# Performance work log

Measured on AMD Instinct MI355X. Metric: run time of the kernel, lower is better.

The kernel has to match this reference:

```python
import jax, jax.numpy as jnp
import numpy as np
from jax import lax

K_TOP = 4
NF1, NF2 = 6, 14
KS1, KS2 = 7, 5


def conv1d_grouped(x, w, b, groups, pad):
    # x: (B, Cin, L), w: (Cout, Cin//groups, K)
    y = lax.conv_general_dilated(x, w, window_strides=(1,), padding=[(pad, pad)],
                                 dimension_numbers=('NCH', 'OIH', 'NCH'),
                                 feature_group_count=groups)
    return y + b[None, :, None]


def kmax_pool(x, k):
    # order-preserving k-max along last axis
    idx = jnp.sort(lax.top_k(x, k)[1], axis=-1)
    return jnp.take_along_axis(x, idx, axis=-1)


def fold_sum(h, b, nf, rows, L):
    # h: (B, rows*nf, L) with group-major channel layout (rows groups of nf)
    h = h.reshape(b, rows, nf, L).transpose(0, 2, 1, 3)        # (B, nf, rows, L)
    h = h.reshape(b, nf, rows // 2, 2, L).sum(axis=3)          # Fold(2,2): sum adjacent row pairs
    return h.transpose(0, 2, 1, 3).reshape(b, (rows // 2) * nf, L)


def setup_inputs() -> dict:
    key = jax.random.key(0)
    ks = jax.random.split(key, 8)
    V, D, C, B, S = 50257, 256, 1000, 32, 1024
    x = jax.random.randint(ks[0], (B, S), 0, V)
    emb = jax.random.normal(ks[1], (V, D), jnp.float32)
    w1 = jax.random.normal(ks[2], (NF1 * D, 1, KS1), jnp.float32) * 0.1
    b1 = jnp.zeros((NF1 * D,), jnp.float32)
    w2 = jax.random.normal(ks[3], (NF2 * (D // 2), NF1, KS2), jnp.float32) * 0.05
    b2 = jnp.zeros((NF2 * (D // 2),), jnp.float32)
    wf = jax.random.normal(ks[4], (C, NF2 * (D // 4) * K_TOP), jnp.float32) * 0.02
    bf = jnp.zeros((C,), jnp.float32)
    return {"x": x, "emb": emb, "w1": w1, "b1": b1, "w2": w2, "b2": b2, "wf": wf, "bf": bf}


def reference(x, emb, w1, b1, w2, b2, wf, bf):
    D = emb.shape[1]
    B = x.shape[0]
    h = emb[x].transpose(0, 2, 1)                 # (B, D, S)
    h = conv1d_grouped(h, w1, b1, groups=D, pad=KS1 - 1)   # (B, 6D, S+6)
    L1 = h.shape[-1]
    h = fold_sum(h, B, NF1, D, L1)                # (B, 3D, L1)
    # dynamic k-max: layer 1 of 2 -> k = max(k_top, ceil(L/2))
    k1 = max(K_TOP, -(-L1 // 2))
    h = jnp.tanh(kmax_pool(h, k1))
    h = conv1d_grouped(h, w2, b2, groups=D // 2, pad=KS2 - 1)  # (B, 7D, k1+4)
    L2 = h.shape[-1]
    h = fold_sum(h, B, NF2, D // 2, L2)           # (B, 14*(D/4), L2)
    h = jnp.tanh(kmax_pool(h, K_TOP))             # (B, 14*(D/4), k_top)
    # dropout is identity in eval mode
    h = h.reshape(B, -1)
    return h @ wf.T + bf
```

## Files before the change

kernel.cpp:

```cpp
#include <hip/hip_runtime.h>
#include <hip/hip_bf16.h>


typedef __attribute__((ext_vector_type(8))) short short8;
typedef __attribute__((ext_vector_type(4))) float f32x4;

__device__ __forceinline__ float fast_tanh(float x) {
    float e = __expf(2.f * x);
    return 1.f - 2.f / (e + 1.f);
}

__device__ __forceinline__ unsigned fkey(float f) {
    unsigned u = __float_as_uint(f);
    return (u & 0x80000000u) ? ~u : (u | 0x80000000u);
}

__device__ __forceinline__ float fkey_inv(unsigned k) {
    unsigned u = (k & 0x80000000u) ? (k ^ 0x80000000u) : ~k;
    return __uint_as_float(u);
}

__device__ __forceinline__ unsigned short f2bf_rne(float f) {
    unsigned u = __float_as_uint(f);
    return (unsigned short)((u + 0x7fffu + ((u >> 16) & 1u)) >> 16);
}

__global__ __launch_bounds__(256) void gather_kernel(
    const int* __restrict__ x, const float* __restrict__ emb, float* __restrict__ E2)
{
    const int b = blockIdx.x >> 4;
    const int c64 = blockIdx.x & 15;
    const int wv = threadIdx.x >> 6, lane = threadIdx.x & 63;
    float* dst = E2 + ((((size_t)b << 6) + lane) << 12);
#pragma unroll
    for (int t = 0; t < 16; ++t) {
        int l = (c64 << 6) + (wv << 4) + t;
        int tok = x[(b << 10) + l];
        float4 v = *(const float4*)(emb + ((size_t)tok << 8) + (lane << 2));
        *(float4*)(dst + (size_t)l * 4) = v;
    }
}

__global__ __launch_bounds__(896) void stage12_kernel(
    const int* __restrict__ x, const float* __restrict__ emb,
    const float* __restrict__ w1, const float* __restrict__ b1,
    const float* __restrict__ w2, const float* __restrict__ b2,
    const float* __restrict__ E2,
    __hip_bfloat16* __restrict__ H)
{
    __shared__ __align__(16) float e[4 * 1104];
    __shared__ __align__(16) float F[12 * 584];
    const int b = blockIdx.x >> 6;
    const int r2 = blockIdx.x & 63;
    const int tid = threadIdx.x;

    for (int i = tid; i < 12 * 584; i += 896) F[i] = 0.f;
    if (E2) {
        const float* E2blk = E2 + ((((size_t)b << 6) + r2) << 12);
        for (int idx = tid; idx < 1104; idx += 896) {
            int l = idx - 6;
            float4 v = {0.f, 0.f, 0.f, 0.f};
            if (l >= 0 && l < 1024) v = *(const float4*)(E2blk + (size_t)l * 4);
            e[0 * 1104 + idx] = v.x; e[1 * 1104 + idx] = v.y;
            e[2 * 1104 + idx] = v.z; e[3 * 1104 + idx] = v.w;
        }
    } else {
        for (int idx = tid; idx < 1104; idx += 896) {
            int l = idx - 6;
            float4 v = {0.f, 0.f, 0.f, 0.f};
            if (l >= 0 && l < 1024) {
                int tok = x[(b << 10) + l];
                v = *(const float4*)(emb + ((size_t)tok << 8) + (r2 << 2));
            }
            e[0 * 1104 + idx] = v.x; e[1 * 1104 + idx] = v.y;
            e[2 * 1104 + idx] = v.z; e[3 * 1104 + idx] = v.w;
        }
    }
    __syncthreads();

    const int w = tid >> 6;
    const int lane = tid & 63;

    if (w < 12) {
        const int half = (w >= 6) ? 1 : 0;
        const int f = w - half * 6;
        const float* ep0 = e + (2 * half) * 1104;
        const float* ep1 = ep0 + 1104;
        const int c0 = __builtin_amdgcn_readfirstlane((2 * (2 * r2 + half)) * 6 + f);
        const int c1 = c0 + 6;
        float wA[7], wB[7];
#pragma unroll
        for (int t = 0; t < 7; ++t) { wA[t] = w1[c0 * 7 + t]; wB[t] = w1[c1 * 7 + t]; }
        const float bias = b1[c0] + b1[c1];

        const int pos0 = lane * 17;
        float a0[7], a1[7];
#pragma unroll
        for (int t = 0; t < 7; ++t) { a0[t] = ep0[pos0 + t]; a1[t] = ep1[pos0 + t]; }

        unsigned key[17];
#pragma unroll
        for (int j = 0; j < 17; ++j) {
            float a = bias;
#pragma unroll
            for (int t = 0; t < 7; ++t) a += a0[t] * wA[t] + a1[t] * wB[t];
            key[j] = (pos0 + j < 1030) ? fkey(a) : 0u;
            if (j < 16) {
#pragma unroll
                for (int t = 0; t < 6; ++t) { a0[t] = a0[t + 1]; a1[t] = a1[t + 1]; }
                a0[6] = ep0[pos0 + j + 7];
                a1[6] = ep1[pos0 + j + 7];
            }
        }

        unsigned T = 0u;
        for (int bit = 31; bit >= 0; --bit) {
            unsigned cand = T | (1u << bit);
            int cnt = 0;
#pragma unroll
            for (int j = 0; j < 17; ++j) cnt += (int)__popcll(__ballot(key[j] >= cand));
            if (cnt >= 515) T = cand;
            if (cnt == 515) break;
        }

        const unsigned long long lm = (1ull << lane) - 1ull;
        int gt_tot = 0, gt_run = 0, eq_run = 0;
#pragma unroll
        for (int j = 0; j < 17; ++j) {
            unsigned long long bg = __ballot(key[j] > T);
            unsigned long long be = __ballot(key[j] == T);
            gt_tot += (int)__popcll(bg);
            gt_run += (int)__popcll(bg & lm);
            eq_run += (int)__popcll(be & lm);
        }
        const int q = 515 - gt_tot;
        float* Frow = F + w * 584;
#pragma unroll
        for (int j = 0; j < 17; ++j) {
            bool isgt = key[j] > T;
            bool iseq = key[j] == T;
            int pos = gt_run + (eq_run < q ? eq_run : q);
            if (isgt || (iseq && eq_run < q)) Frow[4 + pos] = fast_tanh(fkey_inv(key[j]));
            gt_run += isgt ? 1 : 0;
            eq_run += iseq ? 1 : 0;
        }
    }
    __syncthreads();

    {
        const int j = w;
        const int base = lane * 9;
        const int bidx = __builtin_amdgcn_readfirstlane((2 * r2) * 14 + j);
        const float bias2 = b2[bidx] + b2[bidx + 14];
        float acc[9];
#pragma unroll
        for (int jj = 0; jj < 9; ++jj) acc[jj] = bias2;

#pragma unroll
        for (int i = 0; i < 12; ++i) {
            const float* Fr = F + i * 584 + base;
            const int cg = 2 * r2 + ((i >= 6) ? 1 : 0);
            const int ii = (i >= 6) ? (i - 6) : i;
            const int widx = __builtin_amdgcn_readfirstlane(((cg * 14 + j) * 6 + ii) * 5);
            float wv[5];
#pragma unroll
            for (int t = 0; t < 5; ++t) wv[t] = w2[widx + t];
            float win[5];
#pragma unroll
            for (int t = 0; t < 5; ++t) win[t] = Fr[t];
#pragma unroll
            for (int jj = 0; jj < 9; ++jj) {
#pragma unroll
                for (int t = 0; t < 5; ++t) acc[jj] += win[t] * wv[t];
                if (jj < 8) {
#pragma unroll
                    for (int t = 0; t < 4; ++t) win[t] = win[t + 1];
                    win[4] = Fr[jj + 5];
                }
            }
        }

        float vv[9];
#pragma unroll
        for (int jj = 0; jj < 9; ++jj) vv[jj] = (base + jj < 519) ? acc[jj] : -INFINITY;
        float sv[4]; int si[4];
#pragma unroll
        for (int it = 0; it < 4; ++it) {
            float m = vv[0]; int mi = base;
#pragma unroll
            for (int jj = 1; jj < 9; ++jj) { if (vv[jj] > m) { m = vv[jj]; mi = base + jj; } }
#pragma unroll
            for (int d = 1; d < 64; d <<= 1) {
                float om = __shfl_xor(m, d, 64);
                int omi = __shfl_xor(mi, d, 64);
                if (om > m || (om == m && omi < mi)) { m = om; mi = omi; }
            }
            sv[it] = m; si[it] = mi;
            int lj = mi - base;
#pragma unroll
            for (int jj = 0; jj < 9; ++jj) if (jj == lj) vv[jj] = -INFINITY;
        }
#define CSWAP(a, bq) { if (si[a] > si[bq]) { int ti = si[a]; si[a] = si[bq]; si[bq] = ti; \
                                             float tv = sv[a]; sv[a] = sv[bq]; sv[bq] = tv; } }
        CSWAP(0, 1) CSWAP(2, 3) CSWAP(0, 2) CSWAP(1, 3) CSWAP(1, 2)
#undef CSWAP
        if (lane == 0) {
            __hip_bfloat16* op = H + (size_t)b * 3584 + (r2 * 14 + j) * 4;
#pragma unroll
            for (int k = 0; k < 4; ++k) op[k] = __float2bfloat16(fast_tanh(sv[k]));
        }
    }
}

__global__ __launch_bounds__(256) void bias_init_kernel(
    const float* __restrict__ bfv, float* __restrict__ out)
{
    int idx = blockIdx.x * 256 + threadIdx.x;
    if (idx < 32000) out[idx] = bfv[idx - (idx / 1000) * 1000];
}

__global__ __launch_bounds__(256) void stage3_kernel(
    const __hip_bfloat16* __restrict__ Hb, const float* __restrict__ wf,
    float* __restrict__ out)
{
    __shared__ __align__(16) float sred[2 * 4 * 256];
    const int nt = blockIdx.x % 63;
    const int kc = blockIdx.x / 63;
    const int w = threadIdx.x >> 6, lane = threadIdx.x & 63;
    const int row = lane & 15, quad = lane >> 4;
    const int c = nt * 16 + row;
    const bool cvalid = (c < 1000);
    const int kofs = kc * 896 + w * 224 + quad * 8;
    const __hip_bfloat16* ap0 = Hb + (size_t)row * 3584 + kofs;
    const __hip_bfloat16* ap1 = ap0 + (size_t)16 * 3584;
    const float* bp = wf + (size_t)(cvalid ? c : 0) * 3584 + kofs;

    f32x4 acc0 = {0.f, 0.f, 0.f, 0.f};
    f32x4 acc1 = {0.f, 0.f, 0.f, 0.f};
#pragma unroll
    for (int it = 0; it < 7; ++it) {
        short8 a0 = *(const short8*)(ap0 + it * 32);
        short8 a1 = *(const short8*)(ap1 + it * 32);
        float4 p0 = *(const float4*)(bp + it * 32);
        float4 p1 = *(const float4*)(bp + it * 32 + 4);
        short8 bfr;
        bfr[0] = (short)f2bf_rne(p0.x); bfr[1] = (short)f2bf_rne(p0.y);
        bfr[2] = (short)f2bf_rne(p0.z); bfr[3] = (short)f2bf_rne(p0.w);
        bfr[4] = (short)f2bf_rne(p1.x); bfr[5] = (short)f2bf_rne(p1.y);
        bfr[6] = (short)f2bf_rne(p1.z); bfr[7] = (short)f2bf_rne(p1.w);
        if (!cvalid) bfr = short8{0, 0, 0, 0, 0, 0, 0, 0};
        acc0 = __builtin_amdgcn_mfma_f32_16x16x32_bf16(a0, bfr, acc0, 0, 0, 0);
        acc1 = __builtin_amdgcn_mfma_f32_16x16x32_bf16(a1, bfr, acc1, 0, 0, 0);
    }
#pragma unroll
    for (int r_ = 0; r_ < 4; ++r_) {
        sred[(0 * 4 + w) * 256 + lane * 4 + r_] = acc0[r_];
        sred[(1 * 4 + w) * 256 + lane * 4 + r_] = acc1[r_];
    }
    __syncthreads();
    if (threadIdx.x < 128) {
        const int mt = threadIdx.x >> 6;
        const int l2 = threadIdx.x & 63;
        const int rr = l2 & 15, qq = l2 >> 4;
        const int cc = nt * 16 + rr;
        if (cc < 1000) {
            const float* sp = sred + mt * 4 * 256;
#pragma unroll
            for (int r_ = 0; r_ < 4; ++r_) {
                float s = sp[0 * 256 + l2 * 4 + r_] + sp[1 * 256 + l2 * 4 + r_]
                        + sp[2 * 256 + l2 * 4 + r_] + sp[3 * 256 + l2 * 4 + r_];
                int brow = mt * 16 + qq * 4 + r_;
                atomicAdd(&out[brow * 1000 + cc], s);
            }
        }
    }
}

extern "C" void kernel_launch(void* const* d_in, const int* in_sizes, int n_in,
                              void* d_out, int out_size, void* d_ws, size_t ws_size,
                              hipStream_t stream) {
    const int* x      = (const int*)d_in[0];
    const float* emb  = (const float*)d_in[1];
    const float* w1   = (const float*)d_in[2];
    const float* b1   = (const float*)d_in[3];
    const float* w2   = (const float*)d_in[4];
    const float* b2   = (const float*)d_in[5];
    const float* wf   = (const float*)d_in[6];
    const float* bfv  = (const float*)d_in[7];

    const size_t E2_BYTES = (size_t)32 * 64 * 1024 * 4 * 4;
    const size_t H_BYTES  = (size_t)32 * 3584 * 2;
    float* E2 = nullptr;
    __hip_bfloat16* H;
    if (ws_size >= E2_BYTES + H_BYTES) {
        E2 = (float*)d_ws;
        H = (__hip_bfloat16*)((char*)d_ws + E2_BYTES);
    } else {
        H = (__hip_bfloat16*)d_ws;
    }

    bias_init_kernel<<<125, 256, 0, stream>>>(bfv, (float*)d_out);
    if (E2) gather_kernel<<<32 * 16, 256, 0, stream>>>(x, emb, E2);
    stage12_kernel<<<32 * 64, 896, 0, stream>>>(x, emb, w1, b1, w2, b2, E2, H);
    stage3_kernel<<<63 * 4, 256, 0, stream>>>(H, wf, (float*)d_out);
}
```

Baseline: 259.8 us.

## Split fused conv/k-max stage into two kernels with global intermediate buffer

Replaces the single large 896-thread stage12 kernel with a conv1+fold+k-max-select kernel (two blocks per row pair, radix-select via ballots) that writes tanh'd selected values to a global workspace, followed by a conv2+fold+top-4 kernel that reads them back. The aim is higher occupancy and better parallelism by using smaller blocks with less shared memory. In exchange it adds a round trip through global memory for the intermediate (about 50 MB) and one more launch. It also halves the gather kernel's per-block work, and the new path runs only when the workspace is large enough.

```diff
diff --git a/kernel.cpp b/kernel.cpp
--- a/kernel.cpp
+++ b/kernel.cpp
@@ -4,6 +4,7 @@
 
 typedef __attribute__((ext_vector_type(8))) short short8;
 typedef __attribute__((ext_vector_type(4))) float f32x4;
+typedef __attribute__((ext_vector_type(2))) float v2f;
 
 __device__ __forceinline__ float fast_tanh(float x) {
     float e = __expf(2.f * x);
@@ -28,16 +29,190 @@
 __global__ __launch_bounds__(256) void gather_kernel(
     const int* __restrict__ x, const float* __restrict__ emb, float* __restrict__ E2)
 {
-    const int b = blockIdx.x >> 4;
-    const int c64 = blockIdx.x & 15;
+    const int b = blockIdx.x >> 5;
+    const int c32 = blockIdx.x & 31;
     const int wv = threadIdx.x >> 6, lane = threadIdx.x & 63;
     float* dst = E2 + ((((size_t)b << 6) + lane) << 12);
 #pragma unroll
-    for (int t = 0; t < 16; ++t) {
-        int l = (c64 << 6) + (wv << 4) + t;
+    for (int t = 0; t < 8; ++t) {
+        int l = (c32 << 5) + (wv << 3) + t;
         int tok = x[(b << 10) + l];
         float4 v = *(const float4*)(emb + ((size_t)tok << 8) + (lane << 2));
         *(float4*)(dst + (size_t)l * 4) = v;
+    }
+}
+
+__global__ __launch_bounds__(384, 8) void convsel_kernel(
+    const float* __restrict__ E2, const float* __restrict__ w1, const float* __restrict__ b1,
+    float* __restrict__ Fg)
+{
+    __shared__ __align__(8) v2f e2[1104];
+    const int b = blockIdx.x >> 7;
+    const int r2 = (blockIdx.x >> 1) & 63;
+    const int half = blockIdx.x & 1;
+    const int tid = threadIdx.x;
+
+    const float* E2blk = E2 + ((((size_t)b << 6) + r2) << 12) + 2 * half;
+    for (int idx = tid; idx < 1104; idx += 384) {
+        int l = idx - 6;
+        v2f v = {0.f, 0.f};
+        if (l >= 0 && l < 1024) {
+            float2 p = *(const float2*)(E2blk + (size_t)l * 4);
+            v = v2f{p.x, p.y};
+        }
+        e2[idx] = v;
+    }
+    __syncthreads();
+
+    const int w = tid >> 6;
+    const int lane = tid & 63;
+    const int c0 = __builtin_amdgcn_readfirstlane((2 * (2 * r2 + half)) * 6 + w);
+    const int c1 = c0 + 6;
+    v2f wp[7];
+#pragma unroll
+    for (int t = 0; t < 7; ++t) wp[t] = v2f{w1[c0 * 7 + t], w1[c1 * 7 + t]};
+    const float bias = b1[c0] + b1[c1];
+
+    const int pos0 = lane * 17;
+    v2f a01[7];
+#pragma unroll
+    for (int t = 0; t < 7; ++t) a01[t] = e2[pos0 + t];
+
+    unsigned key[17];
+#pragma unroll
+    for (int j = 0; j < 17; ++j) {
+        v2f pa = {0.f, 0.f};
+#pragma unroll
+        for (int t = 0; t < 7; ++t) pa += a01[t] * wp[t];
+        float a = bias + (pa.x + pa.y);
+        key[j] = (pos0 + j < 1030) ? fkey(a) : 0u;
+        if (j < 16) {
+#pragma unroll
+            for (int t = 0; t < 6; ++t) a01[t] = a01[t + 1];
+            a01[6] = e2[pos0 + j + 7];
+        }
+    }
+
+    unsigned T = 0u;
+    for (int bit = 31; bit >= 0; --bit) {
+        unsigned cand = T | (1u << bit);
+        int cnt = 0;
+#pragma unroll
+        for (int j = 0; j < 17; ++j) cnt += (int)__popcll(__ballot(key[j] >= cand));
+        if (cnt >= 515) T = cand;
+        if (cnt == 515) break;
+    }
+
+    const unsigned long long lm = (1ull << lane) - 1ull;
+    int gt_tot = 0, gt_run = 0, eq_run = 0;
+#pragma unroll
+    for (int j = 0; j < 17; ++j) {
+        unsigned long long bg = __ballot(key[j] > T);
+        unsigned long long be = __ballot(key[j] == T);
+        gt_tot += (int)__popcll(bg);
+        gt_run += (int)__popcll(bg & lm);
+        eq_run += (int)__popcll(be & lm);
+    }
+    const int q = 515 - gt_tot;
+    float* Frow = Fg + (size_t)(((b << 6) + r2) * 12 + (half * 6 + w)) * 515;
+#pragma unroll
+    for (int j = 0; j < 17; ++j) {
+        bool isgt = key[j] > T;
+        bool iseq = key[j] == T;
+        int pos = gt_run + (eq_run < q ? eq_run : q);
+        if (isgt || (iseq && eq_run < q)) Frow[pos] = fast_tanh(fkey_inv(key[j]));
+        gt_run += isgt ? 1 : 0;
+        eq_run += iseq ? 1 : 0;
+    }
+}
+
+__global__ __launch_bounds__(448, 7) void conv2max_kernel(
+    const float* __restrict__ Fg, const float* __restrict__ w2, const float* __restrict__ b2,
+    __hip_bfloat16* __restrict__ H)
+{
+    __shared__ __align__(16) float Fs[12 * 584];
+    const int b = blockIdx.x >> 6;
+    const int r2 = blockIdx.x & 63;
+    const int tid = threadIdx.x;
+    const float* Ft = Fg + (size_t)(((b << 6) + r2) * 12) * 515;
+
+#pragma unroll
+    for (int i = 0; i < 12; ++i) {
+        for (int pos = tid; pos < 584; pos += 448) {
+            float v = 0.f;
+            if (pos >= 4 && pos < 519) v = Ft[i * 515 + pos - 4];
+            Fs[i * 584 + pos] = v;
+        }
+    }
+    __syncthreads();
+
+    const int w = tid >> 6;
+    const int lane = tid & 63;
+
+    for (int rep = 0; rep < 2; ++rep) {
+        const int j = w + rep * 7;
+        const int base = lane * 9;
+        const int bidx = __builtin_amdgcn_readfirstlane((2 * r2) * 14 + j);
+        const float bias2 = b2[bidx] + b2[bidx + 14];
+        v2f acc2[9];
+#pragma unroll
+        for (int jj = 0; jj < 9; ++jj) acc2[jj] = v2f{0.f, 0.f};
+
+#pragma unroll
+        for (int pr = 0; pr < 6; ++pr) {
+            const float* Fr0 = Fs + pr * 584 + base;
+            const float* Fr1 = Fr0 + 6 * 584;
+            const int wi0 = __builtin_amdgcn_readfirstlane(((2 * r2) * 14 + j) * 30 + pr * 5);
+            const int wi1 = __builtin_amdgcn_readfirstlane(((2 * r2 + 1) * 14 + j) * 30 + pr * 5);
+            v2f wv2[5], win2[5];
+#pragma unroll
+            for (int t = 0; t < 5; ++t) wv2[t] = v2f{w2[wi0 + t], w2[wi1 + t]};
+#pragma unroll
+            for (int t = 0; t < 5; ++t) win2[t] = v2f{Fr0[t], Fr1[t]};
+#pragma unroll
+            for (int jj = 0; jj < 9; ++jj) {
+#pragma unroll
+                for (int t = 0; t < 5; ++t) acc2[jj] += win2[t] * wv2[t];
+                if (jj < 8) {
+#pragma unroll
+                    for (int t = 0; t < 4; ++t) win2[t] = win2[t + 1];
+                    win2[4] = v2f{Fr0[jj + 5], Fr1[jj + 5]};
+                }
+            }
+        }
+
+        float vv[9];
+#pragma unroll
+        for (int jj = 0; jj < 9; ++jj) {
+            float a = bias2 + (acc2[jj].x + acc2[jj].y);
+            vv[jj] = (base + jj < 519) ? a : -INFINITY;
+        }
+        float sv[4]; int si[4];
+#pragma unroll
+        for (int it = 0; it < 4; ++it) {
+            float m = vv[0]; int mi = base;
+#pragma unroll
+            for (int jj = 1; jj < 9; ++jj) { if (vv[jj] > m) { m = vv[jj]; mi = base + jj; } }
+#pragma unroll
+            for (int d = 1; d < 64; d <<= 1) {
+                float om = __shfl_xor(m, d, 64);
+                int omi = __shfl_xor(mi, d, 64);
+                if (om > m || (om == m && omi < mi)) { m = om; mi = omi; }
+            }
+            sv[it] = m; si[it] = mi;
+            int lj = mi - base;
+#pragma unroll
+            for (int jj = 0; jj < 9; ++jj) if (jj == lj) vv[jj] = -INFINITY;
+        }
+#define CSWAP(a, bq) { if (si[a] > si[bq]) { int ti = si[a]; si[a] = si[bq]; si[bq] = ti; \
+                                             float tv = sv[a]; sv[a] = sv[bq]; sv[bq] = tv; } }
+        CSWAP(0, 1) CSWAP(2, 3) CSWAP(0, 2) CSWAP(1, 3) CSWAP(1, 2)
+#undef CSWAP
+        if (lane == 0) {
+            __hip_bfloat16* op = H + (size_t)b * 3584 + (r2 * 14 + j) * 4;
+#pragma unroll
+            for (int k = 0; k < 4; ++k) op[k] = __float2bfloat16(fast_tanh(sv[k]));
+        }
     }
 }
 
@@ -45,8 +220,7 @@
     const int* __restrict__ x, const float* __restrict__ emb,
     const float* __restrict__ w1, const float* __restrict__ b1,
     const float* __restrict__ w2, const float* __restrict__ b2,
-    const float* __restrict__ E2,
-    __hip_bfloat16* __restrict__ H)
+    const float* __restrict__ E2, __hip_bfloat16* __restrict__ H)
 {
     __shared__ __align__(16) float e[4 * 1104];
     __shared__ __align__(16) float F[12 * 584];
@@ -289,18 +463,28 @@
     const float* bfv  = (const float*)d_in[7];
 
     const size_t E2_BYTES = (size_t)32 * 64 * 1024 * 4 * 4;
+    const size_t F_BYTES  = (size_t)32 * 64 * 12 * 515 * 4;
     const size_t H_BYTES  = (size_t)32 * 3584 * 2;
-    float* E2 = nullptr;
-    __hip_bfloat16* H;
-    if (ws_size >= E2_BYTES + H_BYTES) {
-        E2 = (float*)d_ws;
-        H = (__hip_bfloat16*)((char*)d_ws + E2_BYTES);
+
+    bias_init_kernel<<<125, 256, 0, stream>>>(bfv, (float*)d_out);
+
+    if (ws_size >= E2_BYTES + F_BYTES + H_BYTES) {
+        float* E2 = (float*)d_ws;
+        float* Fg = (float*)((char*)d_ws + E2_BYTES);
+        __hip_bfloat16* H = (__hip_bfloat16*)((char*)d_ws + E2_BYTES + F_BYTES);
+        gather_kernel<<<32 * 32, 256, 0, stream>>>(x, emb, E2);
+        convsel_kernel<<<32 * 64 * 2, 384, 0, stream>>>(E2, w1, b1, Fg);
+        conv2max_kernel<<<32 * 64, 448, 0, stream>>>(Fg, w2, b2, H);
+        stage3_kernel<<<63 * 4, 256, 0, stream>>>(H, wf, (float*)d_out);
+    } else if (ws_size >= E2_BYTES + H_BYTES) {
+        float* E2 = (float*)d_ws;
+        __hip_bfloat16* H = (__hip_bfloat16*)((char*)d_ws + E2_BYTES);
+        gather_kernel<<<32 * 32, 256, 0, stream>>>(x, emb, E2);
+        stage12_kernel<<<32 * 64, 896, 0, stream>>>(x, emb, w1, b1, w2, b2, E2, H);
+        stage3_kernel<<<63 * 4, 256, 0, stream>>>(H, wf, (float*)d_out);
     } else {
-        H = (__hip_bfloat16*)d_ws;
-    }
-
-    bias_init_kernel<<<125, 256, 0, stream>>>(bfv, (float*)d_out);
-    if (E2) gather_kernel<<<32 * 16, 256, 0, stream>>>(x, emb, E2);
-    stage12_kernel<<<32 * 64, 896, 0, stream>>>(x, emb, w1, b1, w2, b2, E2, H);
-    stage3_kernel<<<63 * 4, 256, 0, stream>>>(H, wf, (float*)d_out);
-}
+        __hip_bfloat16* H = (__hip_bfloat16*)d_ws;
+        stage12_kernel<<<32 * 64, 896, 0, stream>>>(x, emb, w1, b1, w2, b2, nullptr, H);
+        stage3_kernel<<<63 * 4, 256, 0, stream>>>(H, wf, (float*)d_out);
+    }
+}
```

After: 352.5 us. +35.7%, slower.
